# Performance work log

Measured on AMD Instinct MI355X. Metric: run time of the kernel, lower is better.

## Reference

```python
import jax, jax.numpy as jnp
import numpy as np

R, C, N, E = 1, 4, 10000, 160000
H, EF, L, OUT = 128, 16, 3, 64


def _gelu(v):
    # torch F.gelu default = exact erf gelu
    return jax.nn.gelu(v, approximate=False)


def setup_inputs() -> dict:
    key = jax.random.key(0)
    ks = jax.random.split(key, 16)
    s = 0.05
    return {
        "x": jax.random.normal(ks[0], (R, C, N, H), jnp.float32),
        "node_mask": jax.random.uniform(ks[1], (R, C, N, 1), jnp.float32),
        "edge_attr": jax.random.normal(ks[2], (E, EF), jnp.float32),
        "bondW": jax.random.normal(ks[3], (EF, H), jnp.float32) * s,
        "bondb": jnp.zeros((H,), jnp.float32),
        "convW1": jax.random.normal(ks[4], (L, H, H), jnp.float32) * s,
        "convb1": jnp.zeros((L, H), jnp.float32),
        "convW2": jax.random.normal(ks[5], (L, H, H), jnp.float32) * s,
        "convb2": jnp.zeros((L, H), jnp.float32),
        "eps": jnp.zeros((L,), jnp.float32),
        "mlpW1": jax.random.normal(ks[6], (H, H), jnp.float32) * s,
        "mlpb1": jnp.zeros((H,), jnp.float32),
        "mlpW2": jax.random.normal(ks[7], (H, OUT), jnp.float32) * s,
        "mlpb2": jnp.zeros((OUT,), jnp.float32),
        "edge_index": jax.random.randint(ks[8], (2, E), 0, N, jnp.int32),
        "batch": jnp.zeros((N,), jnp.int32),
    }


def reference(x, node_mask, edge_attr, bondW, bondb, convW1, convb1, convW2, convb2,
              eps, mlpW1, mlpb1, mlpW2, mlpb2, edge_index, batch):
    src, dst = edge_index[0], edge_index[1]
    # shared bond encoder (Linear), broadcast to [1,1,E,H]
    edge_emb = edge_attr @ bondW + bondb                      # [E, H]
    # edge_weight = node_mask gathered at both endpoints      # [R, C, E, 1]
    edge_mask = node_mask[:, :, src, :] * node_mask[:, :, dst, :]
    for l in range(L):
        # gather-add-GELU-weight-scatter message passing
        msg = _gelu(x[:, :, src, :] + edge_emb) * edge_mask   # [R, C, E, H]
        agg = jnp.zeros_like(x).at[:, :, dst, :].add(msg)     # scatter_sum over dst
        h = (1.0 + eps[l]) * x + agg
        # conv mlp: Linear -> GELU -> Linear
        h = _gelu(h @ convW1[l] + convb1[l]) @ convW2[l] + convb2[l]
        h = _gelu(h)  # outer activation (norm=Identity, dropout=0)
        x = x + h     # residual
    # final MLP (num_mlp_layers=2, PyG MLP default relu act)
    y = jax.nn.relu(x @ mlpW1 + mlpb1) @ mlpW2 + mlpb2        # [R, C, N, OUT]
    denom = jax.lax.stop_gradient(node_mask).sum(axis=2)      # [R, C, 1]
    out = (y * node_mask).sum(axis=2) / denom                 # [R, C, OUT]
    return out
```

## Files before the change

### kernel.cpp

```cpp
#include <hip/hip_runtime.h>
#include <hip/hip_bf16.h>
#include <cstddef>
#include <cstdint>

#define NNODES 10000
#define NEDGES 160000
#define NH     128
#define NCOMBO 4
#define NMROWS (NCOMBO * NNODES)
#define FTILE  32
#define SSTR   136
#define FTILES (NMROWS / FTILE)

typedef __attribute__((ext_vector_type(8))) short short8v;
typedef __attribute__((ext_vector_type(4))) float f32x4;

__device__ __forceinline__ float gelu_f(float v) {
    const float u  = v * 0.70710678118654752f;
    float au = __builtin_fabsf(u);
    au = fminf(au, 3.9192f);
    const float t  = __builtin_amdgcn_rcpf(__builtin_fmaf(0.3275911f, au, 1.0f));
    const float e  = __builtin_amdgcn_exp2f(au * au * -1.4426950408889634f);
    float p = __builtin_fmaf(1.061405429f, t, -1.453152027f);
    p = __builtin_fmaf(p, t, 1.421413741f);
    p = __builtin_fmaf(p, t, -0.284496736f);
    p = __builtin_fmaf(p, t, 0.254829592f);
    const float erf_abs = 1.0f - p * t * e;
    const float erf_s   = __builtin_copysignf(erf_abs, v);
    return 0.5f * v * (1.0f + erf_s);
}

__device__ __forceinline__ uint16_t f2bf_rne(float f) {
    const uint32_t x = __float_as_uint(f);
    return (uint16_t)((x + 0x7fffu + ((x >> 16) & 1u)) >> 16);
}

__global__ __launch_bounds__(256) void hist_kernel(const int* __restrict__ ei,
                                                   int* __restrict__ deg) {
    const int e = blockIdx.x * 256 + threadIdx.x;
    if (e < NEDGES) atomicAdd(&deg[ei[NEDGES + e]], 1);
}

__global__ __launch_bounds__(1024) void scan_kernel(const int* __restrict__ deg,
                                                    int* __restrict__ off,
                                                    int* __restrict__ cursor) {
    __shared__ int ssum[1024];
    const int tid  = threadIdx.x;
    const int base = tid * 10;
    int loc[10];
    int s = 0;
    #pragma unroll
    for (int i = 0; i < 10; ++i) {
        const int idx = base + i;
        loc[i] = s;
        s += (idx < NNODES) ? deg[idx] : 0;
    }
    ssum[tid] = s;
    for (int d = 1; d < 1024; d <<= 1) {
        __syncthreads();
        const int t = (tid >= d) ? ssum[tid - d] : 0;
        __syncthreads();
        ssum[tid] += t;
    }
    __syncthreads();
    const int pref = ssum[tid] - s;
    #pragma unroll
    for (int i = 0; i < 10; ++i) {
        const int idx = base + i;
        if (idx < NNODES) { off[idx] = pref + loc[i]; cursor[idx] = pref + loc[i]; }
    }
    if (tid == 0) off[NNODES] = NEDGES;
}

__global__ __launch_bounds__(256) void scatter_kernel(const int* __restrict__ ei,
                                                      const float* __restrict__ ea,
                                                      int* __restrict__ cursor,
                                                      int* __restrict__ esrc,
                                                      float* __restrict__ ea_s) {
    const int e = blockIdx.x * 256 + threadIdx.x;
    if (e < NEDGES) {
        const int src = ei[e];
        const int dst = ei[NEDGES + e];
        const int pos = atomicAdd(&cursor[dst], 1);
        esrc[pos] = src;
        const float4* s = reinterpret_cast<const float4*>(ea + (size_t)e * 16);
        float4*       d = reinterpret_cast<float4*>(ea_s + (size_t)pos * 16);
        d[0] = s[0]; d[1] = s[1]; d[2] = s[2]; d[3] = s[3];
    }
}

__global__ __launch_bounds__(256) void emb_kernel(
    const float* __restrict__ ea_s, const float* __restrict__ bW,
    const float* __restrict__ bb, uint32_t* __restrict__ embq)
{
    const int lane = threadIdx.x & 63;
    const int wid  = threadIdx.x >> 6;
    const int c0   = lane * 2;
    float2 wc[16];
    #pragma unroll
    for (int k = 0; k < 16; ++k)
        wc[k] = *reinterpret_cast<const float2*>(&bW[k * 128 + c0]);
    const float2 bbr = *reinterpret_cast<const float2*>(&bb[c0]);

    for (int j = blockIdx.x * 4 + wid; j < NEDGES; j += gridDim.x * 4) {
        const float4* eap = reinterpret_cast<const float4*>(ea_s + (size_t)j * 16);
        const float4 a0 = eap[0], a1 = eap[1], a2 = eap[2], a3 = eap[3];
        float s0 = bbr.x, s1 = bbr.y;
        s0 += a0.x*wc[0].x + a0.y*wc[1].x + a0.z*wc[2].x + a0.w*wc[3].x
            + a1.x*wc[4].x + a1.y*wc[5].x + a1.z*wc[6].x + a1.w*wc[7].x
            + a2.x*wc[8].x + a2.y*wc[9].x + a2.z*wc[10].x + a2.w*wc[11].x
            + a3.x*wc[12].x + a3.y*wc[13].x + a3.z*wc[14].x + a3.w*wc[15].x;
        s1 += a0.x*wc[0].y + a0.y*wc[1].y + a0.z*wc[2].y + a0.w*wc[3].y
            + a1.x*wc[4].y + a1.y*wc[5].y + a1.z*wc[6].y + a1.w*wc[7].y
            + a2.x*wc[8].y + a2.y*wc[9].y + a2.z*wc[10].y + a2.w*wc[11].y
            + a3.x*wc[12].y + a3.y*wc[13].y + a3.z*wc[14].y + a3.w*wc[15].y;
        embq[(size_t)j * 64 + lane] =
            ((uint32_t)f2bf_rne(s1) << 16) | (uint32_t)f2bf_rne(s0);
    }
}

__global__ __launch_bounds__(256) void wtrans_kernel(
    const float* __restrict__ cW1, const float* __restrict__ cW2,
    const float* __restrict__ mW1, const float* __restrict__ mW2,
    short* __restrict__ wbf)
{
    const int gidx = blockIdx.x * 256 + threadIdx.x;
    if (gidx >= 122880) return;
    if (gidx < 114688) {
        const int m  = gidx >> 14;
        const int el = gidx & 16383;
        const int n  = el >> 7;
        const int k  = el & 127;
        const float* W = (m < 3) ? (cW1 + m * 16384)
                       : (m < 6) ? (cW2 + (m - 3) * 16384) : mW1;
        wbf[(size_t)m * 16384 + n * 128 + k] = (short)f2bf_rne(W[k * 128 + n]);
    } else {
        const int el = gidx - 114688;
        const int n  = el >> 7;
        const int k  = el & 127;
        wbf[114688 + n * 128 + k] = (short)f2bf_rne(mW2[k * 64 + n]);
    }
}

__global__ __launch_bounds__(256) void agg2_kernel(
    const float* __restrict__ xsrc, const float* __restrict__ nm,
    const uint32_t* __restrict__ embq, const int* __restrict__ off,
    const int* __restrict__ esrc, const float* __restrict__ epsp, int layer,
    float* __restrict__ hout)
{
    const int lane = threadIdx.x & 63;
    const int wid  = threadIdx.x >> 6;
    const int c0   = lane * 2;
    const float epv = 1.0f + epsp[layer];

    for (int n = blockIdx.x * 4 + wid; n < NNODES; n += gridDim.x * 4) {
        const int j0 = off[n], j1 = off[n + 1];
        float dm[4];
        #pragma unroll
        for (int c = 0; c < 4; ++c) dm[c] = nm[c * NNODES + n];

        float acc[4][2] = {{0.f,0.f},{0.f,0.f},{0.f,0.f},{0.f,0.f}};

        uint32_t eqA = 0, eqB = 0;
        float mvA[4], mvB[4]; float2 xvA[4], xvB[4];

#define PF(EQ, MV, XV, JJ)                                                   \
        {                                                                    \
            const int s_ = esrc[(JJ)];                                       \
            EQ = embq[(size_t)(JJ) * 64 + lane];                             \
            _Pragma("unroll")                                                \
            for (int c = 0; c < 4; ++c) {                                    \
                MV[c] = nm[c * NNODES + s_] * dm[c];                         \
                XV[c] = *reinterpret_cast<const float2*>(                    \
                            &xsrc[((size_t)c * NNODES + s_) * NH + c0]);     \
            }                                                                \
        }
#define CONSUME(EQ, MV, XV)                                                  \
        {                                                                    \
            const float e0_ = __uint_as_float(EQ << 16);                     \
            const float e1_ = __uint_as_float(EQ & 0xffff0000u);             \
            _Pragma("unroll")                                                \
            for (int c = 0; c < 4; ++c) {                                    \
                acc[c][0] += gelu_f(XV[c].x + e0_) * MV[c];                  \
                acc[c][1] += gelu_f(XV[c].y + e1_) * MV[c];                  \
            }                                                                \
        }

        if (j0 < j1)     PF(eqA, mvA, xvA, j0);
        if (j0 + 1 < j1) PF(eqB, mvB, xvB, j0 + 1);
        int j = j0;
        while (j < j1) {
            CONSUME(eqA, mvA, xvA);
            if (j + 2 < j1) PF(eqA, mvA, xvA, j + 2);
            ++j;
            if (j >= j1) break;
            CONSUME(eqB, mvB, xvB);
            if (j + 2 < j1) PF(eqB, mvB, xvB, j + 2);
            ++j;
        }
#undef PF
#undef CONSUME

        #pragma unroll
        for (int c = 0; c < 4; ++c) {
            const float2 xo = *reinterpret_cast<const float2*>(
                                  &xsrc[((size_t)c * NNODES + n) * NH + c0]);
            float2 o;
            o.x = epv * xo.x + acc[c][0];
            o.y = epv * xo.y + acc[c][1];
            *reinterpret_cast<float2*>(&hout[((size_t)c * NNODES + n) * NH + c0]) = o;
        }
    }
}

__global__ __launch_bounds__(256) void agg_kernel(
    const float* __restrict__ xcur, const float* __restrict__ nm,
    const float* __restrict__ ea_s, const float* __restrict__ bW,
    const float* __restrict__ bb, const int* __restrict__ off,
    const int* __restrict__ esrc, const float* __restrict__ epsp, int layer,
    float* __restrict__ hout)
{
    const int tid = threadIdx.x;
    const int h   = tid & 127;
    const int sub = tid >> 7;
    float wc[16];
    #pragma unroll
    for (int k = 0; k < 16; ++k) wc[k] = bW[k * 128 + h];
    const float bbr = bb[h];
    const float epv = 1.0f + epsp[layer];

    for (int n = blockIdx.x * 2 + sub; n < NNODES; n += gridDim.x * 2) {
        float acc0 = 0.f, acc1 = 0.f, acc2 = 0.f, acc3 = 0.f;
        const int j0 = off[n], j1 = off[n + 1];
        const float d0 = nm[0*NNODES+n], d1 = nm[1*NNODES+n];
        const float d2 = nm[2*NNODES+n], d3 = nm[3*NNODES+n];
        for (int j = j0; j < j1; ++j) {
            const int src = esrc[j];
            const float4* eap = reinterpret_cast<const float4*>(ea_s + (size_t)j * 16);
            const float4 a0 = eap[0], a1 = eap[1], a2 = eap[2], a3 = eap[3];
            float emb = bbr;
            emb += a0.x*wc[0] + a0.y*wc[1] + a0.z*wc[2] + a0.w*wc[3];
            emb += a1.x*wc[4] + a1.y*wc[5] + a1.z*wc[6] + a1.w*wc[7];
            emb += a2.x*wc[8] + a2.y*wc[9] + a2.z*wc[10] + a2.w*wc[11];
            emb += a3.x*wc[12] + a3.y*wc[13] + a3.z*wc[14] + a3.w*wc[15];
            const float m0 = nm[0*NNODES+src]*d0, m1 = nm[1*NNODES+src]*d1;
            const float m2 = nm[2*NNODES+src]*d2, m3 = nm[3*NNODES+src]*d3;
            acc0 += gelu_f(xcur[((size_t)0*NNODES+src)*NH+h] + emb) * m0;
            acc1 += gelu_f(xcur[((size_t)1*NNODES+src)*NH+h] + emb) * m1;
            acc2 += gelu_f(xcur[((size_t)2*NNODES+src)*NH+h] + emb) * m2;
            acc3 += gelu_f(xcur[((size_t)3*NNODES+src)*NH+h] + emb) * m3;
        }
        hout[((size_t)0*NNODES+n)*NH+h] = epv * xcur[((size_t)0*NNODES+n)*NH+h] + acc0;
        hout[((size_t)1*NNODES+n)*NH+h] = epv * xcur[((size_t)1*NNODES+n)*NH+h] + acc1;
        hout[((size_t)2*NNODES+n)*NH+h] = epv * xcur[((size_t)2*NNODES+n)*NH+h] + acc2;
        hout[((size_t)3*NNODES+n)*NH+h] = epv * xcur[((size_t)3*NNODES+n)*NH+h] + acc3;
    }
}

__global__ __launch_bounds__(256) void conv_mfma_kernel(
    const float* __restrict__ h, const float* __restrict__ resid,
    const short* __restrict__ W1t, const float* __restrict__ b1,
    const short* __restrict__ W2t, const float* __restrict__ b2,
    float* __restrict__ outp)
{
    __shared__ short sh[FTILE * SSTR];
    __shared__ short st[FTILE * SSTR];
    __shared__ short sw[128 * SSTR];

    const int tid  = threadIdx.x;
    const int lane = tid & 63;
    const int w    = tid >> 6;
    const int l15  = lane & 15;
    const int l4   = lane >> 4;
    const int colb = w * 32;
    const int row0 = blockIdx.x * FTILE;

    for (int i = tid; i < FTILE * 32; i += 256) {
        const int r = i >> 5, q = i & 31;
        const float4 v = reinterpret_cast<const float4*>(h + (size_t)(row0 + r) * NH)[q];
        uint2 pk;
        pk.x = ((uint32_t)f2bf_rne(v.y) << 16) | (uint32_t)f2bf_rne(v.x);
        pk.y = ((uint32_t)f2bf_rne(v.w) << 16) | (uint32_t)f2bf_rne(v.z);
        *reinterpret_cast<uint2*>(&sh[r * SSTR + q * 4]) = pk;
    }
    for (int i = tid; i < 128 * 16; i += 256) {
        const int r = i >> 4, c = i & 15;
        *reinterpret_cast<uint4*>(&sw[r * SSTR + c * 8]) =
            *reinterpret_cast<const uint4*>(&W1t[r * 128 + c * 8]);
    }
    __syncthreads();

    f32x4 a00 = {0,0,0,0}, a01 = {0,0,0,0}, a10 = {0,0,0,0}, a11 = {0,0,0,0};
    #pragma unroll
    for (int s = 0; s < 4; ++s) {
        const int ko = s * 32 + l4 * 8;
        short8v fa0 = *reinterpret_cast<const short8v*>(&sh[(l15)      * SSTR + ko]);
        short8v fa1 = *reinterpret_cast<const short8v*>(&sh[(16 + l15) * SSTR + ko]);
        short8v fb0 = *reinterpret_cast<const short8v*>(&sw[(colb + l15)      * SSTR + ko]);
        short8v fb1 = *reinterpret_cast<const short8v*>(&sw[(colb + 16 + l15) * SSTR + ko]);
        a00 = __builtin_amdgcn_mfma_f32_16x16x32_bf16(fa0, fb0, a00, 0, 0, 0);
        a01 = __builtin_amdgcn_mfma_f32_16x16x32_bf16(fa0, fb1, a01, 0, 0, 0);
        a10 = __builtin_amdgcn_mfma_f32_16x16x32_bf16(fa1, fb0, a10, 0, 0, 0);
        a11 = __builtin_amdgcn_mfma_f32_16x16x32_bf16(fa1, fb1, a11, 0, 0, 0);
    }

    {
        const float bv0 = b1[colb + l15];
        const float bv1 = b1[colb + 16 + l15];
        #pragma unroll
        for (int j = 0; j < 4; ++j) {
            const int r0 = l4 * 4 + j;
            st[r0 * SSTR + colb + l15]             = (short)f2bf_rne(gelu_f(a00[j] + bv0));
            st[r0 * SSTR + colb + 16 + l15]        = (short)f2bf_rne(gelu_f(a01[j] + bv1));
            st[(16 + r0) * SSTR + colb + l15]      = (short)f2bf_rne(gelu_f(a10[j] + bv0));
            st[(16 + r0) * SSTR + colb + 16 + l15] = (short)f2bf_rne(gelu_f(a11[j] + bv1));
        }
    }
    __syncthreads();

    for (int i = tid; i < 128 * 16; i += 256) {
        const int r = i >> 4, c = i & 15;
        *reinterpret_cast<uint4*>(&sw[r * SSTR + c * 8]) =
            *reinterpret_cast<const uint4*>(&W2t[r * 128 + c * 8]);
    }
    __syncthreads();

    a00 = {0,0,0,0}; a01 = {0,0,0,0}; a10 = {0,0,0,0}; a11 = {0,0,0,0};
    #pragma unroll
    for (int s = 0; s < 4; ++s) {
        const int ko = s * 32 + l4 * 8;
        short8v fa0 = *reinterpret_cast<const short8v*>(&st[(l15)      * SSTR + ko]);
        short8v fa1 = *reinterpret_cast<const short8v*>(&st[(16 + l15) * SSTR + ko]);
        short8v fb0 = *reinterpret_cast<const short8v*>(&sw[(colb + l15)      * SSTR + ko]);
        short8v fb1 = *reinterpret_cast<const short8v*>(&sw[(colb + 16 + l15) * SSTR + ko]);
        a00 = __builtin_amdgcn_mfma_f32_16x16x32_bf16(fa0, fb0, a00, 0, 0, 0);
        a01 = __builtin_amdgcn_mfma_f32_16x16x32_bf16(fa0, fb1, a01, 0, 0, 0);
        a10 = __builtin_amdgcn_mfma_f32_16x16x32_bf16(fa1, fb0, a10, 0, 0, 0);
        a11 = __builtin_amdgcn_mfma_f32_16x16x32_bf16(fa1, fb1, a11, 0, 0, 0);
    }

    {
        const float bv0 = b2[colb + l15];
        const float bv1 = b2[colb + 16 + l15];
        #pragma unroll
        for (int j = 0; j < 4; ++j) {
            const int r0 = row0 + l4 * 4 + j;
            const int r1 = r0 + 16;
            const size_t o00 = (size_t)r0 * NH + colb + l15;
            const size_t o01 = (size_t)r0 * NH + colb + 16 + l15;
            const size_t o10 = (size_t)r1 * NH + colb + l15;
            const size_t o11 = (size_t)r1 * NH + colb + 16 + l15;
            outp[o00] = resid[o00] + gelu_f(a00[j] + bv0);
            outp[o01] = resid[o01] + gelu_f(a01[j] + bv1);
            outp[o10] = resid[o10] + gelu_f(a10[j] + bv0);
            outp[o11] = resid[o11] + gelu_f(a11[j] + bv1);
        }
    }
}

__global__ __launch_bounds__(256) void mlp_mfma_kernel(
    const float* __restrict__ x,
    const short* __restrict__ W1t, const float* __restrict__ b1,
    const short* __restrict__ W2t,
    const float* __restrict__ b2,
    const float* __restrict__ nm,
    float* __restrict__ oacc)
{
    __shared__ short sx[FTILE * SSTR];
    __shared__ short st[FTILE * SSTR];
    __shared__ short sw[128 * SSTR];
    __shared__ float sacc[256];

    const int tid  = threadIdx.x;
    const int lane = tid & 63;
    const int w    = tid >> 6;
    const int l15  = lane & 15;
    const int l4   = lane >> 4;
    const int colb = w * 32;
    const int row0 = blockIdx.x * FTILE;

    sacc[tid] = 0.0f;

    for (int i = tid; i < FTILE * 32; i += 256) {
        const int r = i >> 5, q = i & 31;
        const float4 v = reinterpret_cast<const float4*>(x + (size_t)(row0 + r) * NH)[q];
        uint2 pk;
        pk.x = ((uint32_t)f2bf_rne(v.y) << 16) | (uint32_t)f2bf_rne(v.x);
        pk.y = ((uint32_t)f2bf_rne(v.w) << 16) | (uint32_t)f2bf_rne(v.z);
        *reinterpret_cast<uint2*>(&sx[r * SSTR + q * 4]) = pk;
    }
    for (int i = tid; i < 128 * 16; i += 256) {
        const int r = i >> 4, c = i & 15;
        *reinterpret_cast<uint4*>(&sw[r * SSTR + c * 8]) =
            *reinterpret_cast<const uint4*>(&W1t[r * 128 + c * 8]);
    }
    __syncthreads();

    f32x4 a00 = {0,0,0,0}, a01 = {0,0,0,0}, a10 = {0,0,0,0}, a11 = {0,0,0,0};
    #pragma unroll
    for (int s = 0; s < 4; ++s) {
        const int ko = s * 32 + l4 * 8;
        short8v fa0 = *reinterpret_cast<const short8v*>(&sx[(l15)      * SSTR + ko]);
        short8v fa1 = *reinterpret_cast<const short8v*>(&sx[(16 + l15) * SSTR + ko]);
        short8v fb0 = *reinterpret_cast<const short8v*>(&sw[(colb + l15)      * SSTR + ko]);
        short8v fb1 = *reinterpret_cast<const short8v*>(&sw[(colb + 16 + l15) * SSTR + ko]);
        a00 = __builtin_amdgcn_mfma_f32_16x16x32_bf16(fa0, fb0, a00, 0, 0, 0);
        a01 = __builtin_amdgcn_mfma_f32_16x16x32_bf16(fa0, fb1, a01, 0, 0, 0);
        a10 = __builtin_amdgcn_mfma_f32_16x16x32_bf16(fa1, fb0, a10, 0, 0, 0);
        a11 = __builtin_amdgcn_mfma_f32_16x16x32_bf16(fa1, fb1, a11, 0, 0, 0);
    }

    {
        const float bv0 = b1[colb + l15];
        const float bv1 = b1[colb + 16 + l15];
        #pragma unroll
        for (int j = 0; j < 4; ++j) {
            const int r0 = l4 * 4 + j;
            st[r0 * SSTR + colb + l15]             = (short)f2bf_rne(fmaxf(a00[j] + bv0, 0.f));
            st[r0 * SSTR + colb + 16 + l15]        = (short)f2bf_rne(fmaxf(a01[j] + bv1, 0.f));
            st[(16 + r0) * SSTR + colb + l15]      = (short)f2bf_rne(fmaxf(a10[j] + bv0, 0.f));
            st[(16 + r0) * SSTR + colb + 16 + l15] = (short)f2bf_rne(fmaxf(a11[j] + bv1, 0.f));
        }
    }
    __syncthreads();

    for (int i = tid; i < 64 * 16; i += 256) {
        const int r = i >> 4, c = i & 15;
        *reinterpret_cast<uint4*>(&sw[r * SSTR + c * 8]) =
            *reinterpret_cast<const uint4*>(&W2t[r * 128 + c * 8]);
    }
    __syncthreads();

    const int colb2 = w * 16;
    f32x4 c0f = {0,0,0,0}, c1f = {0,0,0,0};
    #pragma unroll
    for (int s = 0; s < 4; ++s) {
        const int ko = s * 32 + l4 * 8;
        short8v fa0 = *reinterpret_cast<const short8v*>(&st[(l15)      * SSTR + ko]);
        short8v fa1 = *reinterpret_cast<const short8v*>(&st[(16 + l15) * SSTR + ko]);
        short8v fb  = *reinterpret_cast<const short8v*>(&sw[(colb2 + l15) * SSTR + ko]);
        c0f = __builtin_amdgcn_mfma_f32_16x16x32_bf16(fa0, fb, c0f, 0, 0, 0);
        c1f = __builtin_amdgcn_mfma_f32_16x16x32_bf16(fa1, fb, c1f, 0, 0, 0);
    }

    {
        const float bv = b2[colb2 + l15];
        #pragma unroll
        for (int j = 0; j < 4; ++j) {
            const int gr0 = row0 + l4 * 4 + j;
            const int gr1 = gr0 + 16;
            const float w0 = nm[gr0];
            const float w1 = nm[gr1];
            const int cb0 = gr0 / NNODES;
            const int cb1 = gr1 / NNODES;
            atomicAdd(&sacc[cb0 * 64 + colb2 + l15], (c0f[j] + bv) * w0);
            atomicAdd(&sacc[cb1 * 64 + colb2 + l15], (c1f[j] + bv) * w1);
        }
    }

    __syncthreads();
    atomicAdd(&oacc[tid], sacc[tid]);
}

__global__ __launch_bounds__(256) void final_kernel(
    const float* __restrict__ acc, const float* __restrict__ nm,
    float* __restrict__ outp)
{
    const int tid  = threadIdx.x;
    const int c    = tid >> 6;
    const int lane = tid & 63;
    float s = 0.f;
    for (int n = lane; n < NNODES; n += 64) s += nm[c * NNODES + n];
    #pragma unroll
    for (int off = 32; off > 0; off >>= 1) s += __shfl_down(s, off, 64);
    const float denom = __shfl(s, 0, 64);
    outp[tid] = acc[tid] / denom;
}

extern "C" void kernel_launch(void* const* d_in, const int* in_sizes, int n_in,
                              void* d_out, int out_size, void* d_ws, size_t ws_size,
                              hipStream_t stream) {
    const float* x    = (const float*)d_in[0];
    const float* nm   = (const float*)d_in[1];
    const float* ea   = (const float*)d_in[2];
    const float* bW   = (const float*)d_in[3];
    const float* bb   = (const float*)d_in[4];
    const float* cW1  = (const float*)d_in[5];
    const float* cb1  = (const float*)d_in[6];
    const float* cW2  = (const float*)d_in[7];
    const float* cb2  = (const float*)d_in[8];
    const float* eps  = (const float*)d_in[9];
    const float* mW1  = (const float*)d_in[10];
    const float* mb1  = (const float*)d_in[11];
    const float* mW2  = (const float*)d_in[12];
    const float* mb2  = (const float*)d_in[13];
    const int*   ei   = (const int*)d_in[14];

    float* ws = (float*)d_ws;
    const bool big = ws_size >= (size_t)23230260ULL * 4ULL;

    if (big) {
        float*    xcur = ws;
        float*    hbuf = ws + 5120000;
        float*    oacc = ws + 10240000;
        float*    ea_s = ws + 10240256;
        short*    wbf  = (short*)ea_s;
        uint32_t* embq = (uint32_t*)(ws + 12800256);
        int*      ib   = (int*)(ws + 23040256);
        int* off = ib; int* cur = ib + 10002; int* deg = ib + 20002;
        int* esrc = ib + 30002;

        hipMemsetAsync(deg, 0, 10000 * 4, stream);
        hist_kernel<<<(NEDGES + 255) / 256, 256, 0, stream>>>(ei, deg);
        scan_kernel<<<1, 1024, 0, stream>>>(deg, off, cur);
        scatter_kernel<<<(NEDGES + 255) / 256, 256, 0, stream>>>(ei, ea, cur, esrc, ea_s);
        emb_kernel<<<10000, 256, 0, stream>>>(ea_s, bW, bb, embq);
        wtrans_kernel<<<480, 256, 0, stream>>>(cW1, cW2, mW1, mW2, wbf);

        for (int l = 0; l < 3; ++l) {
            const float* xs = (l == 0) ? x : xcur;
            agg2_kernel<<<2500, 256, 0, stream>>>(xs, nm, embq, off, esrc, eps, l, hbuf);
            conv_mfma_kernel<<<FTILES, 256, 0, stream>>>(hbuf, xs,
                wbf + (size_t)l * 16384, cb1 + l * 128,
                wbf + (size_t)(3 + l) * 16384, cb2 + l * 128, xcur);
        }
        hipMemsetAsync(oacc, 0, 256 * 4, stream);
        mlp_mfma_kernel<<<FTILES, 256, 0, stream>>>(xcur, wbf + 98304, mb1,
                                                    wbf + 114688, mb2, nm, oacc);
        final_kernel<<<1, 256, 0, stream>>>(oacc, nm, (float*)d_out);
    } else {
        float* xcur = ws;
        float* hbuf = ws + 5120000;
        float* oacc = ws + 10240000;
        float* ea_s = ws + 10240256;
        int*   ib   = (int*)(ws + 12800256);
        int* off = ib; int* cur = ib + 10002; int* deg = ib + 20002;
        int* esrc = ib + 30002;
        short* wbf = (short*)(ib + 190004);

        hipMemsetAsync(deg, 0, 10000 * 4, stream);
        hist_kernel<<<(NEDGES + 255) / 256, 256, 0, stream>>>(ei, deg);
        scan_kernel<<<1, 1024, 0, stream>>>(deg, off, cur);
        scatter_kernel<<<(NEDGES + 255) / 256, 256, 0, stream>>>(ei, ea, cur, esrc, ea_s);
        wtrans_kernel<<<480, 256, 0, stream>>>(cW1, cW2, mW1, mW2, wbf);

        for (int l = 0; l < 3; ++l) {
            const float* xs = (l == 0) ? x : xcur;
            agg_kernel<<<2500, 256, 0, stream>>>(xs, nm, ea_s, bW, bb, off, esrc,
                                                 eps, l, hbuf);
            conv_mfma_kernel<<<FTILES, 256, 0, stream>>>(hbuf, xs,
                wbf + (size_t)l * 16384, cb1 + l * 128,
                wbf + (size_t)(3 + l) * 16384, cb2 + l * 128, xcur);
        }
        hipMemsetAsync(oacc, 0, 256 * 4, stream);
        mlp_mfma_kernel<<<FTILES, 256, 0, stream>>>(xcur, wbf + 98304, mb1,
                                                    wbf + 114688, mb2, nm, oacc);
        final_kernel<<<1, 256, 0, stream>>>(oacc, nm, (float*)d_out);
    }
}
```

Before: 452.4 us.

## Store node features and aggregation output as bf16 to halve gather traffic

Adds a bf16 shadow copy of node features, written by a new cast kernel for the first layer and by the conv kernel's epilogue afterwards. The aggregation kernel now gathers bf16 source rows and writes its output in bf16, and the conv and MLP kernels load the pre-packed bf16 tiles directly instead of converting from fp32. This cuts bytes moved in the gather-heavy aggregation and in the intermediate buffer. The cost is an extra cast kernel, extra bf16 stores in conv, and reduced precision in the message inputs; the prefetch depth also drops from two edges to one.

```diff
diff --git a/kernel.cpp b/kernel.cpp
--- a/kernel.cpp
+++ b/kernel.cpp
@@ -34,6 +34,11 @@
     const uint32_t x = __float_as_uint(f);
     return (uint16_t)((x + 0x7fffu + ((x >> 16) & 1u)) >> 16);
 }
+__device__ __forceinline__ uint32_t packbf2(float lo, float hi) {
+    return ((uint32_t)f2bf_rne(hi) << 16) | (uint32_t)f2bf_rne(lo);
+}
+__device__ __forceinline__ float bflo(uint32_t u) { return __uint_as_float(u << 16); }
+__device__ __forceinline__ float bfhi(uint32_t u) { return __uint_as_float(u & 0xffff0000u); }
 
 __global__ __launch_bounds__(256) void hist_kernel(const int* __restrict__ ei,
                                                    int* __restrict__ deg) {
@@ -114,8 +119,7 @@
             + a1.x*wc[4].y + a1.y*wc[5].y + a1.z*wc[6].y + a1.w*wc[7].y
             + a2.x*wc[8].y + a2.y*wc[9].y + a2.z*wc[10].y + a2.w*wc[11].y
             + a3.x*wc[12].y + a3.y*wc[13].y + a3.z*wc[14].y + a3.w*wc[15].y;
-        embq[(size_t)j * 64 + lane] =
-            ((uint32_t)f2bf_rne(s1) << 16) | (uint32_t)f2bf_rne(s0);
+        embq[(size_t)j * 64 + lane] = packbf2(s0, s1);
     }
 }
 
@@ -142,15 +146,26 @@
     }
 }
 
+__global__ __launch_bounds__(256) void xcast_kernel(const float* __restrict__ x,
+                                                    uint32_t* __restrict__ xbf) {
+    const int i = blockIdx.x * 256 + threadIdx.x;
+    if (i < NMROWS * 64) {
+        const float2 v = *reinterpret_cast<const float2*>(&x[(size_t)i * 2]);
+        xbf[i] = packbf2(v.x, v.y);
+    }
+}
+
 __global__ __launch_bounds__(256) void agg2_kernel(
-    const float* __restrict__ xsrc, const float* __restrict__ nm,
-    const uint32_t* __restrict__ embq, const int* __restrict__ off,
-    const int* __restrict__ esrc, const float* __restrict__ epsp, int layer,
-    float* __restrict__ hout)
+    const uint32_t* __restrict__ xbf,
+    const float* __restrict__ nm,
+    const uint32_t* __restrict__ embq,
+    const int*   __restrict__ off,
+    const int*   __restrict__ esrc,
+    const float* __restrict__ epsp, int layer,
+    uint32_t* __restrict__ hbf)
 {
     const int lane = threadIdx.x & 63;
     const int wid  = threadIdx.x >> 6;
-    const int c0   = lane * 2;
     const float epv = 1.0f + epsp[layer];
 
     for (int n = blockIdx.x * 4 + wid; n < NNODES; n += gridDim.x * 4) {
@@ -161,54 +176,44 @@
 
         float acc[4][2] = {{0.f,0.f},{0.f,0.f},{0.f,0.f},{0.f,0.f}};
 
-        uint32_t eqA = 0, eqB = 0;
-        float mvA[4], mvB[4]; float2 xvA[4], xvB[4];
-
-#define PF(EQ, MV, XV, JJ)                                                   \
-        {                                                                    \
-            const int s_ = esrc[(JJ)];                                       \
-            EQ = embq[(size_t)(JJ) * 64 + lane];                             \
-            _Pragma("unroll")                                                \
-            for (int c = 0; c < 4; ++c) {                                    \
-                MV[c] = nm[c * NNODES + s_] * dm[c];                         \
-                XV[c] = *reinterpret_cast<const float2*>(                    \
-                            &xsrc[((size_t)c * NNODES + s_) * NH + c0]);     \
-            }                                                                \
-        }
-#define CONSUME(EQ, MV, XV)                                                  \
-        {                                                                    \
-            const float e0_ = __uint_as_float(EQ << 16);                     \
-            const float e1_ = __uint_as_float(EQ & 0xffff0000u);             \
-            _Pragma("unroll")                                                \
-            for (int c = 0; c < 4; ++c) {                                    \
-                acc[c][0] += gelu_f(XV[c].x + e0_) * MV[c];                  \
-                acc[c][1] += gelu_f(XV[c].y + e1_) * MV[c];                  \
-            }                                                                \
-        }
-
-        if (j0 < j1)     PF(eqA, mvA, xvA, j0);
-        if (j0 + 1 < j1) PF(eqB, mvB, xvB, j0 + 1);
-        int j = j0;
-        while (j < j1) {
-            CONSUME(eqA, mvA, xvA);
-            if (j + 2 < j1) PF(eqA, mvA, xvA, j + 2);
-            ++j;
-            if (j >= j1) break;
-            CONSUME(eqB, mvB, xvB);
-            if (j + 2 < j1) PF(eqB, mvB, xvB, j + 2);
-            ++j;
-        }
-#undef PF
-#undef CONSUME
-
+        uint32_t eq_c = 0; float mv_c[4]; uint32_t xu_c[4];
+        if (j0 < j1) {
+            const int s = esrc[j0];
+            eq_c = embq[(size_t)j0 * 64 + lane];
+            #pragma unroll
+            for (int c = 0; c < 4; ++c) {
+                mv_c[c] = nm[c * NNODES + s] * dm[c];
+                xu_c[c] = xbf[((size_t)c * NNODES + s) * 64 + lane];
+            }
+        }
+        for (int j = j0; j < j1; ++j) {
+            const uint32_t eq = eq_c;
+            float mv[4]; uint32_t xu[4];
+            #pragma unroll
+            for (int c = 0; c < 4; ++c) { mv[c] = mv_c[c]; xu[c] = xu_c[c]; }
+            if (j + 1 < j1) {
+                const int s = esrc[j + 1];
+                eq_c = embq[(size_t)(j + 1) * 64 + lane];
+                #pragma unroll
+                for (int c = 0; c < 4; ++c) {
+                    mv_c[c] = nm[c * NNODES + s] * dm[c];
+                    xu_c[c] = xbf[((size_t)c * NNODES + s) * 64 + lane];
+                }
+            }
+            const float e0 = bflo(eq);
+            const float e1 = bfhi(eq);
+            #pragma unroll
+            for (int c = 0; c < 4; ++c) {
+                acc[c][0] += gelu_f(bflo(xu[c]) + e0) * mv[c];
+                acc[c][1] += gelu_f(bfhi(xu[c]) + e1) * mv[c];
+            }
+        }
         #pragma unroll
         for (int c = 0; c < 4; ++c) {
-            const float2 xo = *reinterpret_cast<const float2*>(
-                                  &xsrc[((size_t)c * NNODES + n) * NH + c0]);
-            float2 o;
-            o.x = epv * xo.x + acc[c][0];
-            o.y = epv * xo.y + acc[c][1];
-            *reinterpret_cast<float2*>(&hout[((size_t)c * NNODES + n) * NH + c0]) = o;
+            const uint32_t u = xbf[((size_t)c * NNODES + n) * 64 + lane];
+            const float o0 = epv * bflo(u) + acc[c][0];
+            const float o1 = epv * bfhi(u) + acc[c][1];
+            hbf[((size_t)c * NNODES + n) * 64 + lane] = packbf2(o0, o1);
         }
     }
 }
@@ -218,7 +223,7 @@
     const float* __restrict__ ea_s, const float* __restrict__ bW,
     const float* __restrict__ bb, const int* __restrict__ off,
     const int* __restrict__ esrc, const float* __restrict__ epsp, int layer,
-    float* __restrict__ hout)
+    short* __restrict__ hbf_s)
 {
     const int tid = threadIdx.x;
     const int h   = tid & 127;
@@ -250,18 +255,20 @@
             acc2 += gelu_f(xcur[((size_t)2*NNODES+src)*NH+h] + emb) * m2;
             acc3 += gelu_f(xcur[((size_t)3*NNODES+src)*NH+h] + emb) * m3;
         }
-        hout[((size_t)0*NNODES+n)*NH+h] = epv * xcur[((size_t)0*NNODES+n)*NH+h] + acc0;
-        hout[((size_t)1*NNODES+n)*NH+h] = epv * xcur[((size_t)1*NNODES+n)*NH+h] + acc1;
-        hout[((size_t)2*NNODES+n)*NH+h] = epv * xcur[((size_t)2*NNODES+n)*NH+h] + acc2;
-        hout[((size_t)3*NNODES+n)*NH+h] = epv * xcur[((size_t)3*NNODES+n)*NH+h] + acc3;
+        hbf_s[((size_t)0*NNODES+n)*NH+h] = (short)f2bf_rne(epv * xcur[((size_t)0*NNODES+n)*NH+h] + acc0);
+        hbf_s[((size_t)1*NNODES+n)*NH+h] = (short)f2bf_rne(epv * xcur[((size_t)1*NNODES+n)*NH+h] + acc1);
+        hbf_s[((size_t)2*NNODES+n)*NH+h] = (short)f2bf_rne(epv * xcur[((size_t)2*NNODES+n)*NH+h] + acc2);
+        hbf_s[((size_t)3*NNODES+n)*NH+h] = (short)f2bf_rne(epv * xcur[((size_t)3*NNODES+n)*NH+h] + acc3);
     }
 }
 
 __global__ __launch_bounds__(256) void conv_mfma_kernel(
-    const float* __restrict__ h, const float* __restrict__ resid,
+    const uint32_t* __restrict__ hb,
+    const float* __restrict__ resid,
     const short* __restrict__ W1t, const float* __restrict__ b1,
     const short* __restrict__ W2t, const float* __restrict__ b2,
-    float* __restrict__ outp)
+    float* __restrict__ outp,
+    short* __restrict__ xb_s)
 {
     __shared__ short sh[FTILE * SSTR];
     __shared__ short st[FTILE * SSTR];
@@ -275,13 +282,10 @@
     const int colb = w * 32;
     const int row0 = blockIdx.x * FTILE;
 
-    for (int i = tid; i < FTILE * 32; i += 256) {
-        const int r = i >> 5, q = i & 31;
-        const float4 v = reinterpret_cast<const float4*>(h + (size_t)(row0 + r) * NH)[q];
-        uint2 pk;
-        pk.x = ((uint32_t)f2bf_rne(v.y) << 16) | (uint32_t)f2bf_rne(v.x);
-        pk.y = ((uint32_t)f2bf_rne(v.w) << 16) | (uint32_t)f2bf_rne(v.z);
-        *reinterpret_cast<uint2*>(&sh[r * SSTR + q * 4]) = pk;
+    for (int i = tid; i < FTILE * 16; i += 256) {
+        const int r = i >> 4, c = i & 15;
+        *reinterpret_cast<uint4*>(&sh[r * SSTR + c * 8]) =
+            *reinterpret_cast<const uint4*>(&hb[(size_t)(row0 + r) * 64 + c * 4]);
     }
     for (int i = tid; i < 128 * 16; i += 256) {
         const int r = i >> 4, c = i & 15;
@@ -350,16 +354,20 @@
             const size_t o01 = (size_t)r0 * NH + colb + 16 + l15;
             const size_t o10 = (size_t)r1 * NH + colb + l15;
             const size_t o11 = (size_t)r1 * NH + colb + 16 + l15;
-            outp[o00] = resid[o00] + gelu_f(a00[j] + bv0);
-            outp[o01] = resid[o01] + gelu_f(a01[j] + bv1);
-            outp[o10] = resid[o10] + gelu_f(a10[j] + bv0);
-            outp[o11] = resid[o11] + gelu_f(a11[j] + bv1);
+            const float v00 = resid[o00] + gelu_f(a00[j] + bv0);
+            const float v01 = resid[o01] + gelu_f(a01[j] + bv1);
+            const float v10 = resid[o10] + gelu_f(a10[j] + bv0);
+            const float v11 = resid[o11] + gelu_f(a11[j] + bv1);
+            outp[o00] = v00; xb_s[o00] = (short)f2bf_rne(v00);
+            outp[o01] = v01; xb_s[o01] = (short)f2bf_rne(v01);
+            outp[o10] = v10; xb_s[o10] = (short)f2bf_rne(v10);
+            outp[o11] = v11; xb_s[o11] = (short)f2bf_rne(v11);
         }
     }
 }
 
 __global__ __launch_bounds__(256) void mlp_mfma_kernel(
-    const float* __restrict__ x,
+    const uint32_t* __restrict__ xb,
     const short* __restrict__ W1t, const float* __restrict__ b1,
     const short* __restrict__ W2t,
     const float* __restrict__ b2,
@@ -381,13 +389,10 @@
 
     sacc[tid] = 0.0f;
 
-    for (int i = tid; i < FTILE * 32; i += 256) {
-        const int r = i >> 5, q = i & 31;
-        const float4 v = reinterpret_cast<const float4*>(x + (size_t)(row0 + r) * NH)[q];
-        uint2 pk;
-        pk.x = ((uint32_t)f2bf_rne(v.y) << 16) | (uint32_t)f2bf_rne(v.x);
-        pk.y = ((uint32_t)f2bf_rne(v.w) << 16) | (uint32_t)f2bf_rne(v.z);
-        *reinterpret_cast<uint2*>(&sx[r * SSTR + q * 4]) = pk;
+    for (int i = tid; i < FTILE * 16; i += 256) {
+        const int r = i >> 4, c = i & 15;
+        *reinterpret_cast<uint4*>(&sx[r * SSTR + c * 8]) =
+            *reinterpret_cast<const uint4*>(&xb[(size_t)(row0 + r) * 64 + c * 4]);
     }
     for (int i = tid; i < 128 * 16; i += 256) {
         const int r = i >> 4, c = i & 15;
@@ -497,16 +502,17 @@
     const int*   ei   = (const int*)d_in[14];
 
     float* ws = (float*)d_ws;
-    const bool big = ws_size >= (size_t)23230260ULL * 4ULL;
+    const bool big = ws_size >= (size_t)23230600ULL * 4ULL;
 
     if (big) {
         float*    xcur = ws;
-        float*    hbuf = ws + 5120000;
-        float*    oacc = ws + 10240000;
-        float*    ea_s = ws + 10240256;
+        float*    oacc = ws + 5120000;
+        uint32_t* hbf  = (uint32_t*)(ws + 5120512);
+        uint32_t* xbf  = (uint32_t*)(ws + 7680512);
+        float*    ea_s = ws + 10240512;
         short*    wbf  = (short*)ea_s;
-        uint32_t* embq = (uint32_t*)(ws + 12800256);
-        int*      ib   = (int*)(ws + 23040256);
+        uint32_t* embq = (uint32_t*)(ws + 12800512);
+        int*      ib   = (int*)(ws + 23040512);
         int* off = ib; int* cur = ib + 10002; int* deg = ib + 20002;
         int* esrc = ib + 30002;
 
@@ -516,28 +522,32 @@
         scatter_kernel<<<(NEDGES + 255) / 256, 256, 0, stream>>>(ei, ea, cur, esrc, ea_s);
         emb_kernel<<<10000, 256, 0, stream>>>(ea_s, bW, bb, embq);
         wtrans_kernel<<<480, 256, 0, stream>>>(cW1, cW2, mW1, mW2, wbf);
+        xcast_kernel<<<10000, 256, 0, stream>>>(x, xbf);
 
         for (int l = 0; l < 3; ++l) {
-            const float* xs = (l == 0) ? x : xcur;
-            agg2_kernel<<<2500, 256, 0, stream>>>(xs, nm, embq, off, esrc, eps, l, hbuf);
-            conv_mfma_kernel<<<FTILES, 256, 0, stream>>>(hbuf, xs,
+            const float* resid = (l == 0) ? x : xcur;
+            agg2_kernel<<<2500, 256, 0, stream>>>(xbf, nm, embq, off, esrc, eps, l, hbf);
+            conv_mfma_kernel<<<FTILES, 256, 0, stream>>>(hbf, resid,
                 wbf + (size_t)l * 16384, cb1 + l * 128,
-                wbf + (size_t)(3 + l) * 16384, cb2 + l * 128, xcur);
+                wbf + (size_t)(3 + l) * 16384, cb2 + l * 128,
+                xcur, (short*)xbf);
         }
         hipMemsetAsync(oacc, 0, 256 * 4, stream);
-        mlp_mfma_kernel<<<FTILES, 256, 0, stream>>>(xcur, wbf + 98304, mb1,
+        mlp_mfma_kernel<<<FTILES, 256, 0, stream>>>(xbf, wbf + 98304, mb1,
                                                     wbf + 114688, mb2, nm, oacc);
         final_kernel<<<1, 256, 0, stream>>>(oacc, nm, (float*)d_out);
     } else {
-        float* xcur = ws;
-        float* hbuf = ws + 5120000;
-        float* oacc = ws + 10240000;
-        float* ea_s = ws + 10240256;
-        int*   ib   = (int*)(ws + 12800256);
+        float*    xcur = ws;
+        float*    oacc = ws + 5120000;
+        uint32_t* hbf  = (uint32_t*)(ws + 5120512);
+        uint32_t* xbf  = (uint32_t*)(ws + 7680512);
+        float*    ea_s = ws + 10240512;
+        int*      ib   = (int*)(ws + 12800512);
         int* off = ib; int* cur = ib + 10002; int* deg = ib + 20002;
         int* esrc = ib + 30002;
         short* wbf = (short*)(ib + 190004);
 
+        hipMemcpyAsync(xcur, x, (size_t)5120000 * 4, hipMemcpyDeviceToDevice, stream);
         hipMemsetAsync(deg, 0, 10000 * 4, stream);
         hist_kernel<<<(NEDGES + 255) / 256, 256, 0, stream>>>(ei, deg);
         scan_kernel<<<1, 1024, 0, stream>>>(deg, off, cur);
@@ -545,15 +555,15 @@
         wtrans_kernel<<<480, 256, 0, stream>>>(cW1, cW2, mW1, mW2, wbf);
 
         for (int l = 0; l < 3; ++l) {
-            const float* xs = (l == 0) ? x : xcur;
-            agg_kernel<<<2500, 256, 0, stream>>>(xs, nm, ea_s, bW, bb, off, esrc,
-                                                 eps, l, hbuf);
-            conv_mfma_kernel<<<FTILES, 256, 0, stream>>>(hbuf, xs,
+            agg_kernel<<<2500, 256, 0, stream>>>(xcur, nm, ea_s, bW, bb, off, esrc,
+                                                 eps, l, (short*)hbf);
+            conv_mfma_kernel<<<FTILES, 256, 0, stream>>>(hbf, xcur,
                 wbf + (size_t)l * 16384, cb1 + l * 128,
-                wbf + (size_t)(3 + l) * 16384, cb2 + l * 128, xcur);
+                wbf + (size_t)(3 + l) * 16384, cb2 + l * 128,
+                xcur, (short*)xbf);
         }
         hipMemsetAsync(oacc, 0, 256 * 4, stream);
-        mlp_mfma_kernel<<<FTILES, 256, 0, stream>>>(xcur, wbf + 98304, mb1,
+        mlp_mfma_kernel<<<FTILES, 256, 0, stream>>>(xbf, wbf + 98304, mb1,
                                                     wbf + 114688, mb2, nm, oacc);
         final_kernel<<<1, 256, 0, stream>>>(oacc, nm, (float*)d_out);
     }
```

Result: faster. 441.8 us (-2.4%).
